# Kernel tuning notes

Measured on AMD Instinct MI355X. Metric: run time of the kernel, lower is better.

## Reference

```python
import jax, jax.numpy as jnp
import numpy as np

EMBED_DICT = 200
EMBED_DIM = 16
HIDDEN = 32
LSTM_DIM = 256
B, C, L = 8192, 16, 64
END_IDX = 1  # stand-in for token_list.index('<End>')


def _lin(k, i, o):
    return jax.random.normal(k, (i, o), jnp.float32) * (1.0 / np.sqrt(i))


def setup_inputs() -> dict:
    key = jax.random.key(0)
    ks = jax.random.split(key, 20)
    feat_in = EMBED_DIM * 14 + LSTM_DIM  # 480
    z = lambda n: jnp.zeros((n,), jnp.float32)
    return {
        "trees": jax.random.randint(ks[0], (B, 1 + C, 17), 0, L),
        "lstm_out_list": jax.random.normal(ks[1], (B, L, 1, LSTM_DIM), jnp.float32),
        "first_notes": jax.random.normal(ks[2], (B, EMBED_DIM), jnp.float32),
        "train": 1,
        "embedding": jax.random.normal(ks[3], (EMBED_DICT, EMBED_DIM), jnp.float32) * 0.05,
        "leaf_end_W": _lin(ks[4], EMBED_DIM, HIDDEN), "leaf_end_b": z(HIDDEN),
        "lc_W1": _lin(ks[5], feat_in, HIDDEN * 4), "lc_b1": z(HIDDEN * 4),
        "lc_W2": _lin(ks[6], HIDDEN * 4, HIDDEN), "lc_b2": z(HIDDEN),
        "cs_W1": _lin(ks[7], HIDDEN * 2, HIDDEN * 4), "cs_b1": z(HIDDEN * 4),
        "cs_W2": _lin(ks[8], HIDDEN * 4, HIDDEN), "cs_b2": z(HIDDEN),
        "nf_W1": _lin(ks[9], feat_in, HIDDEN * 4), "nf_b1": z(HIDDEN * 4),
        "nf_W2": _lin(ks[10], HIDDEN * 4, HIDDEN), "nf_b2": z(HIDDEN),
        "cb_W1": _lin(ks[11], HIDDEN * 2, HIDDEN * 4), "cb_b1": z(HIDDEN * 4),
        "cb_W2": _lin(ks[12], HIDDEN * 4, HIDDEN), "cb_b2": z(HIDDEN),
        "ff_W1": _lin(ks[13], HIDDEN, HIDDEN), "ff_b1": z(HIDDEN),
        "ff_W2": _lin(ks[14], HIDDEN, HIDDEN), "ff_b2": z(HIDDEN),
        "ts_W": _lin(ks[15], HIDDEN, 1), "ts_b": z(1),
    }


def _mlp2(x, W1, b1, W2, b2):
    # Linear -> ReLU -> Linear -> ReLU (matches nn.Sequential blocks)
    return jax.nn.relu(jax.nn.relu(x @ W1 + b1) @ W2 + b2)


def reference(trees, lstm_out_list, first_notes, train, embedding,
              leaf_end_W, leaf_end_b, lc_W1, lc_b1, lc_W2, lc_b2,
              cs_W1, cs_b1, cs_W2, cs_b2, nf_W1, nf_b1, nf_W2, nf_b2,
              cb_W1, cb_b1, cb_W2, cb_b2, ff_W1, ff_b1, ff_W2, ff_b2,
              ts_W, ts_b):
    Bn = trees.shape[0]
    root = trees[:, 0, :]        # (B, 17)
    leaves = trees[:, 1:, :]     # (B, C, 17)
    Cn = leaves.shape[1]
    bidx = jnp.arange(Bn)

    # ---- leaf nodes: either leaf_end_ff(embed(type)) or leaf_child_ff(concat) ----
    leaf_tok = embedding[leaves[:, :, 2:-1]].reshape(Bn, Cn, -1)       # (B,C,224)
    leaf_ptr = lstm_out_list[bidx[:, None], leaves[:, :, -1], 0, :]    # (B,C,256)
    leaf_child = _mlp2(jnp.concatenate([leaf_tok, leaf_ptr], -1),
                       lc_W1, lc_b1, lc_W2, lc_b2)                     # (B,C,32)
    leaf_end = embedding[leaves[:, :, 2]] @ leaf_end_W + leaf_end_b    # (B,C,32)
    is_end = (leaves[:, :, 2] == END_IDX)[..., None]
    children = jnp.where(is_end, leaf_end, leaf_child)                 # (B,C,32)

    # ---- sequential left fold with child_sum_ff over children ----
    def step(carry, child):
        nxt = _mlp2(jnp.concatenate([carry, child], -1), cs_W1, cs_b1, cs_W2, cs_b2)
        return nxt, None
    child_summary, _ = jax.lax.scan(step, children[:, 0],
                                    jnp.moveaxis(children[:, 1:], 0, 1))  # (B,32)

    # ---- root node embedding + combine ----
    node_tok = embedding[root[:, 2:-1]].reshape(Bn, -1)                # (B,224)
    node_ptr = lstm_out_list[bidx, root[:, -1], 0, :]                  # (B,256)
    node_tmp = _mlp2(jnp.concatenate([node_tok, node_ptr], -1),
                     nf_W1, nf_b1, nf_W2, nf_b2)                       # (B,32)
    tree_sum = _mlp2(jnp.concatenate([node_tmp, child_summary], -1),
                     cb_W1, cb_b1, cb_W2, cb_b2)                       # (B,32)

    # ---- head: two linears (no activation) then score ----
    ff = (tree_sum @ ff_W1 + ff_b1) @ ff_W2 + ff_b2
    return ff @ ts_W + ts_b                                            # (B,1)
```

## Files before the change

### kernel.cpp

```cpp
#include <hip/hip_runtime.h>
#include <cstddef>


typedef __bf16 bf16x8 __attribute__((ext_vector_type(8)));
typedef __bf16 bf16x4 __attribute__((ext_vector_type(4)));
typedef float  f32x4  __attribute__((ext_vector_type(4)));

__global__ __launch_bounds__(256) void prep_kernel(
    const float* __restrict__ embedding,
    const float* __restrict__ leaf_end_W, const float* __restrict__ leaf_end_b,
    const float* __restrict__ lc_W1, const float* __restrict__ lc_W2,
    const float* __restrict__ nf_W1, const float* __restrict__ nf_W2,
    const float* __restrict__ cs_W1, const float* __restrict__ cs_W2,
    const float* __restrict__ cb_W1, const float* __restrict__ cb_W2,
    const float* __restrict__ ff_W1, const float* __restrict__ ff_b1,
    const float* __restrict__ ff_W2, const float* __restrict__ ff_b2,
    const float* __restrict__ ts_W, const float* __restrict__ ts_b,
    __bf16* __restrict__ lcW1T, __bf16* __restrict__ nfW1T,
    __bf16* __restrict__ lcW2T, __bf16* __restrict__ nfW2T,
    __bf16* __restrict__ emb_bf, float* __restrict__ endvec,
    __bf16* __restrict__ csW1Th, __bf16* __restrict__ csW1Tl,
    __bf16* __restrict__ cbW1Th, __bf16* __restrict__ cbW1Tl,
    __bf16* __restrict__ csW2Th, __bf16* __restrict__ csW2Tl,
    __bf16* __restrict__ cbW2Th, __bf16* __restrict__ cbW2Tl,
    float* __restrict__ vfin, float* __restrict__ cfin)
{
    const int id = blockIdx.x * 256 + threadIdx.x;
    if (id < 61440) {
        const int n = id / 480, k = id - n * 480;
        lcW1T[id] = (__bf16)lc_W1[k * 128 + n];
    } else if (id < 122880) {
        const int e = id - 61440;
        const int n = e / 480, k = e - n * 480;
        nfW1T[e] = (__bf16)nf_W1[k * 128 + n];
    } else if (id < 126976) {
        const int e = id - 122880;
        const int n = e / 128, k = e - n * 128;
        lcW2T[e] = (__bf16)lc_W2[k * 32 + n];
    } else if (id < 131072) {
        const int e = id - 126976;
        const int n = e / 128, k = e - n * 128;
        nfW2T[e] = (__bf16)nf_W2[k * 32 + n];
    } else if (id < 134272) {
        emb_bf[id - 131072] = (__bf16)embedding[id - 131072];
    } else if (id < 134304) {
        const int c = id - 134272;
        float a = leaf_end_b[c];
        #pragma unroll
        for (int d = 0; d < 16; ++d) a = fmaf(embedding[16 + d], leaf_end_W[d * 32 + c], a);
        endvec[c] = a;
    } else if (id < 142496) {
        const int e = id - 134304;
        const int n = e >> 6, k = e & 63;
        const float v = cs_W1[k * 128 + n];
        const __bf16 h = (__bf16)v;
        csW1Th[e] = h; csW1Tl[e] = (__bf16)(v - (float)h);
    } else if (id < 150688) {
        const int e = id - 142496;
        const int n = e >> 6, k = e & 63;
        const float v = cb_W1[k * 128 + n];
        const __bf16 h = (__bf16)v;
        cbW1Th[e] = h; cbW1Tl[e] = (__bf16)(v - (float)h);
    } else if (id < 154784) {
        const int e = id - 150688;
        const int n = e >> 7, k = e & 127;
        const float v = cs_W2[k * 32 + n];
        const __bf16 h = (__bf16)v;
        csW2Th[e] = h; csW2Tl[e] = (__bf16)(v - (float)h);
    } else if (id < 158880) {
        const int e = id - 154784;
        const int n = e >> 7, k = e & 127;
        const float v = cb_W2[k * 32 + n];
        const __bf16 h = (__bf16)v;
        cbW2Th[e] = h; cbW2Tl[e] = (__bf16)(v - (float)h);
    } else if (id < 158912) {
        const int c = id - 158880;
        float w2t[32];
        #pragma unroll
        for (int k = 0; k < 32; ++k) {
            float a = 0.f;
            for (int j = 0; j < 32; ++j) a = fmaf(ff_W2[k * 32 + j], ts_W[j], a);
            w2t[k] = a;
        }
        float a = 0.f;
        #pragma unroll
        for (int k = 0; k < 32; ++k) a = fmaf(ff_W1[c * 32 + k], w2t[k], a);
        vfin[c] = a;
    } else if (id == 158912) {
        float a = ts_b[0];
        for (int j = 0; j < 32; ++j) a = fmaf(ff_b2[j], ts_W[j], a);
        for (int k = 0; k < 32; ++k) {
            float w2t = 0.f;
            for (int j = 0; j < 32; ++j) w2t = fmaf(ff_W2[k * 32 + j], ts_W[j], w2t);
            a = fmaf(ff_b1[k], w2t, a);
        }
        cfin[0] = a;
    }
}

__global__ __launch_bounds__(256, 4) void mlp1_mfma(
    const int* __restrict__ trees,
    const float* __restrict__ lstm,
    const __bf16* __restrict__ lcW1T, const __bf16* __restrict__ nfW1T,
    const __bf16* __restrict__ lcW2T, const __bf16* __restrict__ nfW2T,
    const __bf16* __restrict__ emb_bf, const float* __restrict__ endvec,
    const float* __restrict__ lc_b1, const float* __restrict__ lc_b2,
    const float* __restrict__ nf_b1, const float* __restrict__ nf_b2,
    __bf16* __restrict__ childrenH, __bf16* __restrict__ childrenL,
    __bf16* __restrict__ node_tmpH, __bf16* __restrict__ node_tmpL)
{
    __shared__ __align__(16) __bf16 emb_s[3200];
    __shared__ __align__(16) __bf16 Hs[64][136];
    __shared__ float b1s[128], b2s[32], evs[32];
    __shared__ int   endf[64];

    const int tid = threadIdx.x;
    const int blk = blockIdx.x;
    const bool leaf = (blk < 2048);

    const __bf16* __restrict__ W1T = leaf ? lcW1T : nfW1T;
    const __bf16* __restrict__ W2T = leaf ? lcW2T : nfW2T;
    const float*  __restrict__ b1p = leaf ? lc_b1 : nf_b1;
    const float*  __restrict__ b2p = leaf ? lc_b2 : nf_b2;

    for (int i = tid; i < 3200; i += 256) emb_s[i] = emb_bf[i];
    if (tid < 128) b1s[tid] = b1p[tid];
    if (tid < 32)  { b2s[tid] = b2p[tid]; evs[tid] = leaf ? endvec[tid] : 0.f; }
    if (tid < 64) {
        if (leaf) {
            const int R = blk * 64 + tid;
            const int b = R >> 4, trow = 1 + (R & 15);
            endf[tid] = (trees[(b * 17 + trow) * 17 + 2] == 1);
        } else endf[tid] = 0;
    }

    const int l  = tid & 63;
    const int w  = tid >> 6;
    const int wm = w >> 1;
    const int wn = w & 1;
    const int lm = l & 15;
    const int kb = l >> 4;

    const int* tb[2];
    const float* lb[2];
    #pragma unroll
    for (int i = 0; i < 2; ++i) {
        const int r = wm * 32 + i * 16 + lm;
        int b, trow;
        if (leaf) { const int R = blk * 64 + r; b = R >> 4; trow = 1 + (R & 15); }
        else      { b = (blk - 2048) * 64 + r; trow = 0; }
        const int* t = trees + (b * 17 + trow) * 17;
        tb[i] = t;
        lb[i] = lstm + ((size_t)b * 64 + (size_t)t[16]) * 256;
    }

    f32x4 acc[2][4];
    #pragma unroll
    for (int i = 0; i < 2; ++i)
        #pragma unroll
        for (int j = 0; j < 4; ++j) acc[i][j] = (f32x4){0.f, 0.f, 0.f, 0.f};

    __syncthreads();

    #pragma unroll
    for (int c = 0; c < 15; ++c) {
        bf16x8 bfr[4];
        #pragma unroll
        for (int ct = 0; ct < 4; ++ct) {
            const int n = wn * 64 + ct * 16 + lm;
            bfr[ct] = *(const bf16x8*)(W1T + n * 480 + c * 32 + kb * 8);
        }
        bf16x8 afr[2];
        if (c < 7) {
            #pragma unroll
            for (int i = 0; i < 2; ++i) {
                const int tok = tb[i][2 + 2 * c + (kb >> 1)];
                afr[i] = *(const bf16x8*)(emb_s + tok * 16 + (kb & 1) * 8);
            }
        } else {
            #pragma unroll
            for (int i = 0; i < 2; ++i) {
                const float* p = lb[i] + (c - 7) * 32 + kb * 8;
                const float4 u = *(const float4*)p;
                const float4 v = *(const float4*)(p + 4);
                bf16x8 t;
                t[0] = (__bf16)u.x; t[1] = (__bf16)u.y; t[2] = (__bf16)u.z; t[3] = (__bf16)u.w;
                t[4] = (__bf16)v.x; t[5] = (__bf16)v.y; t[6] = (__bf16)v.z; t[7] = (__bf16)v.w;
                afr[i] = t;
            }
        }
        #pragma unroll
        for (int i = 0; i < 2; ++i)
            #pragma unroll
            for (int ct = 0; ct < 4; ++ct)
                acc[i][ct] = __builtin_amdgcn_mfma_f32_16x16x32_bf16(afr[i], bfr[ct], acc[i][ct], 0, 0, 0);
    }

    #pragma unroll
    for (int i = 0; i < 2; ++i)
        #pragma unroll
        for (int ct = 0; ct < 4; ++ct) {
            const int col = wn * 64 + ct * 16 + lm;
            const float bias = b1s[col];
            #pragma unroll
            for (int rg = 0; rg < 4; ++rg) {
                float v = acc[i][ct][rg] + bias;
                v = v > 0.f ? v : 0.f;
                Hs[wm * 32 + i * 16 + 4 * kb + rg][col] = (__bf16)v;
            }
        }
    __syncthreads();

    f32x4 acc2[2];
    acc2[0] = (f32x4){0.f, 0.f, 0.f, 0.f};
    acc2[1] = (f32x4){0.f, 0.f, 0.f, 0.f};

    #pragma unroll
    for (int kc = 0; kc < 4; ++kc) {
        const bf16x8 a2 = *(const bf16x8*)(&Hs[w * 16 + lm][kc * 32 + kb * 8]);
        #pragma unroll
        for (int j = 0; j < 2; ++j) {
            const bf16x8 b2 = *(const bf16x8*)(W2T + (j * 16 + lm) * 128 + kc * 32 + kb * 8);
            acc2[j] = __builtin_amdgcn_mfma_f32_16x16x32_bf16(a2, b2, acc2[j], 0, 0, 0);
        }
    }

    #pragma unroll
    for (int j = 0; j < 2; ++j) {
        const int col = j * 16 + lm;
        const float bias = b2s[col];
        #pragma unroll
        for (int rg = 0; rg < 4; ++rg) {
            const int row = w * 16 + 4 * kb + rg;
            float v = acc2[j][rg] + bias;
            v = v > 0.f ? v : 0.f;
            if (leaf && endf[row]) v = evs[col];
            const __bf16 h  = (__bf16)v;
            const __bf16 lo = (__bf16)(v - (float)h);
            if (leaf) {
                const size_t R = (size_t)blk * 64 + row;
                childrenH[R * 32 + col] = h;
                childrenL[R * 32 + col] = lo;
            } else {
                const size_t R = (size_t)(blk - 2048) * 64 + row;
                node_tmpH[R * 32 + col] = h;
                node_tmpL[R * 32 + col] = lo;
            }
        }
    }
}

__global__ __launch_bounds__(256) void scan_mfma(
    const __bf16* __restrict__ childrenH, const __bf16* __restrict__ childrenL,
    const __bf16* __restrict__ node_tmpH, const __bf16* __restrict__ node_tmpL,
    const __bf16* __restrict__ csW1Th, const __bf16* __restrict__ csW1Tl,
    const __bf16* __restrict__ csW2Th, const __bf16* __restrict__ csW2Tl,
    const __bf16* __restrict__ cbW1Th, const __bf16* __restrict__ cbW1Tl,
    const __bf16* __restrict__ cbW2Th, const __bf16* __restrict__ cbW2Tl,
    const float* __restrict__ cs_b1, const float* __restrict__ cs_b2,
    const float* __restrict__ cb_b1, const float* __restrict__ cb_b2,
    const float* __restrict__ vfin_g, const float* __restrict__ cfin_g,
    float* __restrict__ out)
{
    __shared__ __align__(16) __bf16 Xh[32][72], Xl[32][72];
    __shared__ __align__(16) __bf16 Hh[32][136], Hl[32][136];
    __shared__ float b1a[128], b1b[128], b2a[32], b2b[32], vfin[32];
    __shared__ float psum[2][32];
    __shared__ float cfin_s;

    const int tid = threadIdx.x;
    const int l = tid & 63, w = tid >> 6;
    const int lm = l & 15, kb = l >> 4;

    if (tid < 128)      { b1a[tid] = cs_b1[tid]; b1b[tid] = cb_b1[tid]; }
    else if (tid < 160) { b2a[tid - 128] = cs_b2[tid - 128]; b2b[tid - 128] = cb_b2[tid - 128]; }
    else if (tid < 192) { vfin[tid - 160] = vfin_g[tid - 160]; }
    else if (tid == 192) cfin_s = cfin_g[0];

    bf16x8 W1r[2][2][2];
    {
        #pragma unroll
        for (int nt = 0; nt < 2; ++nt)
            #pragma unroll
            for (int kc = 0; kc < 2; ++kc) {
                const int n = w * 32 + nt * 16 + lm;
                W1r[nt][kc][0] = *(const bf16x8*)(csW1Th + n * 64 + kc * 32 + kb * 8);
                W1r[nt][kc][1] = *(const bf16x8*)(csW1Tl + n * 64 + kc * 32 + kb * 8);
            }
    }
    bf16x8 W2r[4][2];
    {
        const int n2 = (w & 1) * 16 + lm;
        #pragma unroll
        for (int kc = 0; kc < 4; ++kc) {
            W2r[kc][0] = *(const bf16x8*)(csW2Th + n2 * 128 + kc * 32 + kb * 8);
            W2r[kc][1] = *(const bf16x8*)(csW2Tl + n2 * 128 + kc * 32 + kb * 8);
        }
    }

    const size_t base = (size_t)blockIdx.x * 32;
    const int tt = tid >> 3, c4 = (tid & 7) * 4;

    {
        const size_t o0 = ((base + tt) * 16 + 0) * 32 + c4;
        const size_t o1 = ((base + tt) * 16 + 1) * 32 + c4;
        *(bf16x4*)&Xh[tt][c4]      = *(const bf16x4*)(childrenH + o0);
        *(bf16x4*)&Xl[tt][c4]      = *(const bf16x4*)(childrenL + o0);
        *(bf16x4*)&Xh[tt][32 + c4] = *(const bf16x4*)(childrenH + o1);
        *(bf16x4*)&Xl[tt][32 + c4] = *(const bf16x4*)(childrenL + o1);
    }
    __syncthreads();

    #pragma unroll 1
    for (int it = 1; it <= 16; ++it) {
        const bool fin = (it == 16);
        if (fin) {
            #pragma unroll
            for (int nt = 0; nt < 2; ++nt)
                #pragma unroll
                for (int kc = 0; kc < 2; ++kc) {
                    const int n = w * 32 + nt * 16 + lm;
                    W1r[nt][kc][0] = *(const bf16x8*)(cbW1Th + n * 64 + kc * 32 + kb * 8);
                    W1r[nt][kc][1] = *(const bf16x8*)(cbW1Tl + n * 64 + kc * 32 + kb * 8);
                }
            const int n2 = (w & 1) * 16 + lm;
            #pragma unroll
            for (int kc = 0; kc < 4; ++kc) {
                W2r[kc][0] = *(const bf16x8*)(cbW2Th + n2 * 128 + kc * 32 + kb * 8);
                W2r[kc][1] = *(const bf16x8*)(cbW2Tl + n2 * 128 + kc * 32 + kb * 8);
            }
        }
        const float* __restrict__ b1c = fin ? b1b : b1a;
        const float* __restrict__ b2c = fin ? b2b : b2a;

        bf16x4 pfh, pfl;
        const int pfmode = (it < 15) ? 1 : (it == 15 ? 2 : 0);
        if (pfmode == 1) {
            const size_t o = ((base + tt) * 16 + (it + 1)) * 32 + c4;
            pfh = *(const bf16x4*)(childrenH + o);
            pfl = *(const bf16x4*)(childrenL + o);
        } else if (pfmode == 2) {
            const size_t o = (base + tt) * 32 + c4;
            pfh = *(const bf16x4*)(node_tmpH + o);
            pfl = *(const bf16x4*)(node_tmpL + o);
        }

        bf16x8 xh[2][2], xl[2][2];
        #pragma unroll
        for (int i = 0; i < 2; ++i)
            #pragma unroll
            for (int kc = 0; kc < 2; ++kc) {
                const int row = i * 16 + lm;
                xh[i][kc] = *(const bf16x8*)&Xh[row][kc * 32 + kb * 8];
                xl[i][kc] = *(const bf16x8*)&Xl[row][kc * 32 + kb * 8];
            }
        f32x4 a1[2][2];
        #pragma unroll
        for (int i = 0; i < 2; ++i)
            #pragma unroll
            for (int nt = 0; nt < 2; ++nt) {
                a1[i][nt] = (f32x4){0.f, 0.f, 0.f, 0.f};
                #pragma unroll
                for (int kc = 0; kc < 2; ++kc) {
                    a1[i][nt] = __builtin_amdgcn_mfma_f32_16x16x32_bf16(xh[i][kc], W1r[nt][kc][0], a1[i][nt], 0, 0, 0);
                    a1[i][nt] = __builtin_amdgcn_mfma_f32_16x16x32_bf16(xl[i][kc], W1r[nt][kc][0], a1[i][nt], 0, 0, 0);
                    a1[i][nt] = __builtin_amdgcn_mfma_f32_16x16x32_bf16(xh[i][kc], W1r[nt][kc][1], a1[i][nt], 0, 0, 0);
                }
            }
        #pragma unroll
        for (int i = 0; i < 2; ++i)
            #pragma unroll
            for (int nt = 0; nt < 2; ++nt) {
                const int col = w * 32 + nt * 16 + lm;
                const float bias = b1c[col];
                #pragma unroll
                for (int rg = 0; rg < 4; ++rg) {
                    const int row = i * 16 + 4 * kb + rg;
                    float v = a1[i][nt][rg] + bias;
                    v = v > 0.f ? v : 0.f;
                    const __bf16 h = (__bf16)v;
                    Hh[row][col] = h;
                    Hl[row][col] = (__bf16)(v - (float)h);
                }
            }
        __syncthreads();

        const int mt = w >> 1;
        f32x4 a2 = (f32x4){0.f, 0.f, 0.f, 0.f};
        #pragma unroll
        for (int kc = 0; kc < 4; ++kc) {
            const bf16x8 ah = *(const bf16x8*)&Hh[mt * 16 + lm][kc * 32 + kb * 8];
            const bf16x8 al = *(const bf16x8*)&Hl[mt * 16 + lm][kc * 32 + kb * 8];
            a2 = __builtin_amdgcn_mfma_f32_16x16x32_bf16(ah, W2r[kc][0], a2, 0, 0, 0);
            a2 = __builtin_amdgcn_mfma_f32_16x16x32_bf16(al, W2r[kc][0], a2, 0, 0, 0);
            a2 = __builtin_amdgcn_mfma_f32_16x16x32_bf16(ah, W2r[kc][1], a2, 0, 0, 0);
        }

        if (!fin) {
            const int cb_ = (it == 15) ? 32 : 0;
            const int col = (w & 1) * 16 + lm;
            const float bias = b2c[col];
            #pragma unroll
            for (int rg = 0; rg < 4; ++rg) {
                const int row = mt * 16 + 4 * kb + rg;
                float v = a2[rg] + bias;
                v = v > 0.f ? v : 0.f;
                const __bf16 h = (__bf16)v;
                Xh[row][cb_ + col] = h;
                Xl[row][cb_ + col] = (__bf16)(v - (float)h);
            }
            if (pfmode) {
                const int dst = (pfmode == 2) ? 0 : 32;
                *(bf16x4*)&Xh[tt][dst + c4] = pfh;
                *(bf16x4*)&Xl[tt][dst + c4] = pfl;
            }
            __syncthreads();
        } else {
            const int col = (w & 1) * 16 + lm;
            const float bias = b2c[col];
            const float vf = vfin[col];
            float part[4];
            #pragma unroll
            for (int rg = 0; rg < 4; ++rg) {
                float v = a2[rg] + bias;
                v = v > 0.f ? v : 0.f;
                part[rg] = v * vf;
            }
            #pragma unroll
            for (int m = 1; m < 16; m <<= 1)
                #pragma unroll
                for (int rg = 0; rg < 4; ++rg)
                    part[rg] += __shfl_xor(part[rg], m, 64);
            if (lm == 0) {
                #pragma unroll
                for (int rg = 0; rg < 4; ++rg)
                    psum[w & 1][mt * 16 + 4 * kb + rg] = part[rg];
            }
            __syncthreads();
            if (tid < 32) out[base + tid] = cfin_s + psum[0][tid] + psum[1][tid];
        }
    }
}

extern "C" void kernel_launch(void* const* d_in, const int* in_sizes, int n_in,
                              void* d_out, int out_size, void* d_ws, size_t ws_size,
                              hipStream_t stream) {
    const int*   trees      = (const int*)d_in[0];
    const float* lstm       = (const float*)d_in[1];
    const float* embedding  = (const float*)d_in[4];
    const float* leaf_end_W = (const float*)d_in[5];
    const float* leaf_end_b = (const float*)d_in[6];
    const float* lc_W1 = (const float*)d_in[7];
    const float* lc_b1 = (const float*)d_in[8];
    const float* lc_W2 = (const float*)d_in[9];
    const float* lc_b2 = (const float*)d_in[10];
    const float* cs_W1 = (const float*)d_in[11];
    const float* cs_b1 = (const float*)d_in[12];
    const float* cs_W2 = (const float*)d_in[13];
    const float* cs_b2 = (const float*)d_in[14];
    const float* nf_W1 = (const float*)d_in[15];
    const float* nf_b1 = (const float*)d_in[16];
    const float* nf_W2 = (const float*)d_in[17];
    const float* nf_b2 = (const float*)d_in[18];
    const float* cb_W1 = (const float*)d_in[19];
    const float* cb_b1 = (const float*)d_in[20];
    const float* cb_W2 = (const float*)d_in[21];
    const float* cb_b2 = (const float*)d_in[22];
    const float* ff_W1 = (const float*)d_in[23];
    const float* ff_b1 = (const float*)d_in[24];
    const float* ff_W2 = (const float*)d_in[25];
    const float* ff_b2 = (const float*)d_in[26];
    const float* ts_W  = (const float*)d_in[27];
    const float* ts_b  = (const float*)d_in[28];

    char* ws = (char*)d_ws;
    __bf16* childrenH = (__bf16*)ws;
    __bf16* childrenL = (__bf16*)(ws + 8388608);
    __bf16* node_tmpH = (__bf16*)(ws + 16777216);
    __bf16* node_tmpL = (__bf16*)(ws + 17301504);
    __bf16* lcW1T    = (__bf16*)(ws + 17825792);
    __bf16* nfW1T    = (__bf16*)(ws + 17948672);
    __bf16* lcW2T    = (__bf16*)(ws + 18071552);
    __bf16* nfW2T    = (__bf16*)(ws + 18079744);
    __bf16* emb_bf   = (__bf16*)(ws + 18087936);
    float*  endvec   = (float*)(ws + 18094336);
    __bf16* csW1Th   = (__bf16*)(ws + 18094464);
    __bf16* csW1Tl   = (__bf16*)(ws + 18110848);
    __bf16* cbW1Th   = (__bf16*)(ws + 18127232);
    __bf16* cbW1Tl   = (__bf16*)(ws + 18143616);
    __bf16* csW2Th   = (__bf16*)(ws + 18160000);
    __bf16* csW2Tl   = (__bf16*)(ws + 18168192);
    __bf16* cbW2Th   = (__bf16*)(ws + 18176384);
    __bf16* cbW2Tl   = (__bf16*)(ws + 18184576);
    float*  vfin     = (float*)(ws + 18192768);
    float*  cfin     = (float*)(ws + 18192896);
    float*  outp     = (float*)d_out;

    prep_kernel<<<dim3(621), dim3(256), 0, stream>>>(
        embedding, leaf_end_W, leaf_end_b, lc_W1, lc_W2, nf_W1, nf_W2,
        cs_W1, cs_W2, cb_W1, cb_W2, ff_W1, ff_b1, ff_W2, ff_b2, ts_W, ts_b,
        lcW1T, nfW1T, lcW2T, nfW2T, emb_bf, endvec,
        csW1Th, csW1Tl, cbW1Th, cbW1Tl, csW2Th, csW2Tl, cbW2Th, cbW2Tl,
        vfin, cfin);

    mlp1_mfma<<<dim3(2176), dim3(256), 0, stream>>>(
        trees, lstm, lcW1T, nfW1T, lcW2T, nfW2T, emb_bf, endvec,
        lc_b1, lc_b2, nf_b1, nf_b2, childrenH, childrenL, node_tmpH, node_tmpL);

    scan_mfma<<<dim3(256), dim3(256), 0, stream>>>(
        childrenH, childrenL, node_tmpH, node_tmpL,
        csW1Th, csW1Tl, csW2Th, csW2Tl, cbW1Th, cbW1Tl, cbW2Th, cbW2Tl,
        cs_b1, cs_b2, cb_b1, cb_b2, vfin, cfin, outp);
}
```

Before: 129.3 us.

## Halve mlp1 tile rows, swap MFMA operands for packed stores, coalesce prep reads

```diff
diff --git a/kernel.cpp b/kernel.cpp
--- a/kernel.cpp
+++ b/kernel.cpp
@@ -27,20 +27,20 @@
 {
     const int id = blockIdx.x * 256 + threadIdx.x;
     if (id < 61440) {
-        const int n = id / 480, k = id - n * 480;
-        lcW1T[id] = (__bf16)lc_W1[k * 128 + n];
+        const int k = id >> 7, n = id & 127;
+        lcW1T[n * 480 + k] = (__bf16)lc_W1[id];
     } else if (id < 122880) {
         const int e = id - 61440;
-        const int n = e / 480, k = e - n * 480;
-        nfW1T[e] = (__bf16)nf_W1[k * 128 + n];
+        const int k = e >> 7, n = e & 127;
+        nfW1T[n * 480 + k] = (__bf16)nf_W1[e];
     } else if (id < 126976) {
         const int e = id - 122880;
-        const int n = e / 128, k = e - n * 128;
-        lcW2T[e] = (__bf16)lc_W2[k * 32 + n];
+        const int k = e >> 5, n = e & 31;
+        lcW2T[n * 128 + k] = (__bf16)lc_W2[e];
     } else if (id < 131072) {
         const int e = id - 126976;
-        const int n = e / 128, k = e - n * 128;
-        nfW2T[e] = (__bf16)nf_W2[k * 32 + n];
+        const int k = e >> 5, n = e & 31;
+        nfW2T[n * 128 + k] = (__bf16)nf_W2[e];
     } else if (id < 134272) {
         emb_bf[id - 131072] = (__bf16)embedding[id - 131072];
     } else if (id < 134304) {
@@ -51,28 +51,28 @@
         endvec[c] = a;
     } else if (id < 142496) {
         const int e = id - 134304;
-        const int n = e >> 6, k = e & 63;
-        const float v = cs_W1[k * 128 + n];
+        const int k = e >> 7, n = e & 127;
+        const float v = cs_W1[e];
         const __bf16 h = (__bf16)v;
-        csW1Th[e] = h; csW1Tl[e] = (__bf16)(v - (float)h);
+        csW1Th[n * 64 + k] = h; csW1Tl[n * 64 + k] = (__bf16)(v - (float)h);
     } else if (id < 150688) {
         const int e = id - 142496;
-        const int n = e >> 6, k = e & 63;
-        const float v = cb_W1[k * 128 + n];
+        const int k = e >> 7, n = e & 127;
+        const float v = cb_W1[e];
         const __bf16 h = (__bf16)v;
-        cbW1Th[e] = h; cbW1Tl[e] = (__bf16)(v - (float)h);
+        cbW1Th[n * 64 + k] = h; cbW1Tl[n * 64 + k] = (__bf16)(v - (float)h);
     } else if (id < 154784) {
         const int e = id - 150688;
-        const int n = e >> 7, k = e & 127;
-        const float v = cs_W2[k * 32 + n];
+        const int k = e >> 5, n = e & 31;
+        const float v = cs_W2[e];
         const __bf16 h = (__bf16)v;
-        csW2Th[e] = h; csW2Tl[e] = (__bf16)(v - (float)h);
+        csW2Th[n * 128 + k] = h; csW2Tl[n * 128 + k] = (__bf16)(v - (float)h);
     } else if (id < 158880) {
         const int e = id - 154784;
-        const int n = e >> 7, k = e & 127;
-        const float v = cb_W2[k * 32 + n];
+        const int k = e >> 5, n = e & 31;
+        const float v = cb_W2[e];
         const __bf16 h = (__bf16)v;
-        cbW2Th[e] = h; cbW2Tl[e] = (__bf16)(v - (float)h);
+        cbW2Th[n * 128 + k] = h; cbW2Tl[n * 128 + k] = (__bf16)(v - (float)h);
     } else if (id < 158912) {
         const int c = id - 158880;
         float w2t[32];
@@ -98,7 +98,7 @@
     }
 }
 
-__global__ __launch_bounds__(256, 4) void mlp1_mfma(
+__global__ __launch_bounds__(256, 6) void mlp1_mfma(
     const int* __restrict__ trees,
     const float* __restrict__ lstm,
     const __bf16* __restrict__ lcW1T, const __bf16* __restrict__ nfW1T,
@@ -110,13 +110,13 @@
     __bf16* __restrict__ node_tmpH, __bf16* __restrict__ node_tmpL)
 {
     __shared__ __align__(16) __bf16 emb_s[3200];
-    __shared__ __align__(16) __bf16 Hs[64][136];
+    __shared__ __align__(16) __bf16 Hs[32][136];
     __shared__ float b1s[128], b2s[32], evs[32];
-    __shared__ int   endf[64];
+    __shared__ int   endf[32];
 
     const int tid = threadIdx.x;
     const int blk = blockIdx.x;
-    const bool leaf = (blk < 2048);
+    const bool leaf = (blk < 4096);
 
     const __bf16* __restrict__ W1T = leaf ? lcW1T : nfW1T;
     const __bf16* __restrict__ W2T = leaf ? lcW2T : nfW2T;
@@ -126,9 +126,9 @@
     for (int i = tid; i < 3200; i += 256) emb_s[i] = emb_bf[i];
     if (tid < 128) b1s[tid] = b1p[tid];
     if (tid < 32)  { b2s[tid] = b2p[tid]; evs[tid] = leaf ? endvec[tid] : 0.f; }
-    if (tid < 64) {
+    if (tid < 32) {
         if (leaf) {
-            const int R = blk * 64 + tid;
+            const int R = blk * 32 + tid;
             const int b = R >> 4, trow = 1 + (R & 15);
             endf[tid] = (trees[(b * 17 + trow) * 17 + 2] == 1);
         } else endf[tid] = 0;
@@ -136,116 +136,95 @@
 
     const int l  = tid & 63;
     const int w  = tid >> 6;
-    const int wm = w >> 1;
-    const int wn = w & 1;
     const int lm = l & 15;
     const int kb = l >> 4;
-
-    const int* tb[2];
-    const float* lb[2];
+    const int rowbase = (w >> 1) * 16;
+    const int colbase = (w & 1) * 64;
+
+    const int row = rowbase + lm;
+    int b, trow;
+    if (leaf) { const int R = blk * 32 + row; b = R >> 4; trow = 1 + (R & 15); }
+    else      { b = (blk - 4096) * 32 + row; trow = 0; }
+    const int* __restrict__ ti = trees + (b * 17 + trow) * 17;
+    const float* __restrict__ lrow = lstm + ((size_t)b * 64 + (size_t)ti[16]) * 256;
+
+    f32x4 acc[4];
     #pragma unroll
-    for (int i = 0; i < 2; ++i) {
-        const int r = wm * 32 + i * 16 + lm;
-        int b, trow;
-        if (leaf) { const int R = blk * 64 + r; b = R >> 4; trow = 1 + (R & 15); }
-        else      { b = (blk - 2048) * 64 + r; trow = 0; }
-        const int* t = trees + (b * 17 + trow) * 17;
-        tb[i] = t;
-        lb[i] = lstm + ((size_t)b * 64 + (size_t)t[16]) * 256;
-    }
-
-    f32x4 acc[2][4];
-    #pragma unroll
-    for (int i = 0; i < 2; ++i)
-        #pragma unroll
-        for (int j = 0; j < 4; ++j) acc[i][j] = (f32x4){0.f, 0.f, 0.f, 0.f};
+    for (int j = 0; j < 4; ++j) acc[j] = (f32x4){0.f, 0.f, 0.f, 0.f};
 
     __syncthreads();
 
     #pragma unroll
     for (int c = 0; c < 15; ++c) {
-        bf16x8 bfr[4];
+        bf16x8 wfr[4];
         #pragma unroll
         for (int ct = 0; ct < 4; ++ct) {
-            const int n = wn * 64 + ct * 16 + lm;
-            bfr[ct] = *(const bf16x8*)(W1T + n * 480 + c * 32 + kb * 8);
-        }
-        bf16x8 afr[2];
+            const int n = colbase + ct * 16 + lm;
+            wfr[ct] = *(const bf16x8*)(W1T + n * 480 + c * 32 + kb * 8);
+        }
+        bf16x8 afr;
         if (c < 7) {
-            #pragma unroll
-            for (int i = 0; i < 2; ++i) {
-                const int tok = tb[i][2 + 2 * c + (kb >> 1)];
-                afr[i] = *(const bf16x8*)(emb_s + tok * 16 + (kb & 1) * 8);
-            }
+            const int tok = ti[2 + 2 * c + (kb >> 1)];
+            afr = *(const bf16x8*)(emb_s + tok * 16 + (kb & 1) * 8);
         } else {
-            #pragma unroll
-            for (int i = 0; i < 2; ++i) {
-                const float* p = lb[i] + (c - 7) * 32 + kb * 8;
-                const float4 u = *(const float4*)p;
-                const float4 v = *(const float4*)(p + 4);
-                bf16x8 t;
-                t[0] = (__bf16)u.x; t[1] = (__bf16)u.y; t[2] = (__bf16)u.z; t[3] = (__bf16)u.w;
-                t[4] = (__bf16)v.x; t[5] = (__bf16)v.y; t[6] = (__bf16)v.z; t[7] = (__bf16)v.w;
-                afr[i] = t;
-            }
-        }
-        #pragma unroll
-        for (int i = 0; i < 2; ++i)
-            #pragma unroll
-            for (int ct = 0; ct < 4; ++ct)
-                acc[i][ct] = __builtin_amdgcn_mfma_f32_16x16x32_bf16(afr[i], bfr[ct], acc[i][ct], 0, 0, 0);
+            const float* p = lrow + (c - 7) * 32 + kb * 8;
+            const float4 u = *(const float4*)p;
+            const float4 v = *(const float4*)(p + 4);
+            bf16x8 t;
+            t[0] = (__bf16)u.x; t[1] = (__bf16)u.y; t[2] = (__bf16)u.z; t[3] = (__bf16)u.w;
+            t[4] = (__bf16)v.x; t[5] = (__bf16)v.y; t[6] = (__bf16)v.z; t[7] = (__bf16)v.w;
+            afr = t;
+        }
+        #pragma unroll
+        for (int ct = 0; ct < 4; ++ct)
+            acc[ct] = __builtin_amdgcn_mfma_f32_16x16x32_bf16(wfr[ct], afr, acc[ct], 0, 0, 0);
     }
 
     #pragma unroll
-    for (int i = 0; i < 2; ++i)
-        #pragma unroll
-        for (int ct = 0; ct < 4; ++ct) {
-            const int col = wn * 64 + ct * 16 + lm;
-            const float bias = b1s[col];
-            #pragma unroll
-            for (int rg = 0; rg < 4; ++rg) {
-                float v = acc[i][ct][rg] + bias;
-                v = v > 0.f ? v : 0.f;
-                Hs[wm * 32 + i * 16 + 4 * kb + rg][col] = (__bf16)v;
-            }
-        }
+    for (int ct = 0; ct < 4; ++ct) {
+        const int wcol = colbase + ct * 16 + 4 * kb;
+        bf16x4 pk;
+        #pragma unroll
+        for (int rg = 0; rg < 4; ++rg) {
+            float v = acc[ct][rg] + b1s[wcol + rg];
+            v = v > 0.f ? v : 0.f;
+            pk[rg] = (__bf16)v;
+        }
+        *(bf16x4*)&Hs[rowbase + lm][wcol] = pk;
+    }
     __syncthreads();
 
-    f32x4 acc2[2];
-    acc2[0] = (f32x4){0.f, 0.f, 0.f, 0.f};
-    acc2[1] = (f32x4){0.f, 0.f, 0.f, 0.f};
-
+    const int mt = w >> 1, jn = w & 1;
+    f32x4 a2 = (f32x4){0.f, 0.f, 0.f, 0.f};
     #pragma unroll
     for (int kc = 0; kc < 4; ++kc) {
-        const bf16x8 a2 = *(const bf16x8*)(&Hs[w * 16 + lm][kc * 32 + kb * 8]);
-        #pragma unroll
-        for (int j = 0; j < 2; ++j) {
-            const bf16x8 b2 = *(const bf16x8*)(W2T + (j * 16 + lm) * 128 + kc * 32 + kb * 8);
-            acc2[j] = __builtin_amdgcn_mfma_f32_16x16x32_bf16(a2, b2, acc2[j], 0, 0, 0);
-        }
-    }
-
-    #pragma unroll
-    for (int j = 0; j < 2; ++j) {
-        const int col = j * 16 + lm;
-        const float bias = b2s[col];
+        const bf16x8 wf = *(const bf16x8*)(W2T + (jn * 16 + lm) * 128 + kc * 32 + kb * 8);
+        const bf16x8 hf = *(const bf16x8*)(&Hs[mt * 16 + lm][kc * 32 + kb * 8]);
+        a2 = __builtin_amdgcn_mfma_f32_16x16x32_bf16(wf, hf, a2, 0, 0, 0);
+    }
+
+    {
+        const int orow = mt * 16 + lm;
+        const int ocol = jn * 16 + 4 * kb;
+        const bool isend = leaf && endf[orow];
+        bf16x4 ph, pl;
         #pragma unroll
         for (int rg = 0; rg < 4; ++rg) {
-            const int row = w * 16 + 4 * kb + rg;
-            float v = acc2[j][rg] + bias;
+            float v = a2[rg] + b2s[ocol + rg];
             v = v > 0.f ? v : 0.f;
-            if (leaf && endf[row]) v = evs[col];
-            const __bf16 h  = (__bf16)v;
-            const __bf16 lo = (__bf16)(v - (float)h);
-            if (leaf) {
-                const size_t R = (size_t)blk * 64 + row;
-                childrenH[R * 32 + col] = h;
-                childrenL[R * 32 + col] = lo;
-            } else {
-                const size_t R = (size_t)(blk - 2048) * 64 + row;
-                node_tmpH[R * 32 + col] = h;
-                node_tmpL[R * 32 + col] = lo;
-            }
+            if (isend) v = evs[ocol + rg];
+            const __bf16 h = (__bf16)v;
+            ph[rg] = h;
+            pl[rg] = (__bf16)(v - (float)h);
+        }
+        if (leaf) {
+            const size_t R = (size_t)blk * 32 + orow;
+            *(bf16x4*)&childrenH[R * 32 + ocol] = ph;
+            *(bf16x4*)&childrenL[R * 32 + ocol] = pl;
+        } else {
+            const size_t R = (size_t)(blk - 4096) * 32 + orow;
+            *(bf16x4*)&node_tmpH[R * 32 + ocol] = ph;
+            *(bf16x4*)&node_tmpL[R * 32 + ocol] = pl;
         }
     }
 }
@@ -278,16 +257,14 @@
     else if (tid == 192) cfin_s = cfin_g[0];
 
     bf16x8 W1r[2][2][2];
-    {
-        #pragma unroll
-        for (int nt = 0; nt < 2; ++nt)
-            #pragma unroll
-            for (int kc = 0; kc < 2; ++kc) {
-                const int n = w * 32 + nt * 16 + lm;
-                W1r[nt][kc][0] = *(const bf16x8*)(csW1Th + n * 64 + kc * 32 + kb * 8);
-                W1r[nt][kc][1] = *(const bf16x8*)(csW1Tl + n * 64 + kc * 32 + kb * 8);
-            }
-    }
+    #pragma unroll
+    for (int nt = 0; nt < 2; ++nt)
+        #pragma unroll
+        for (int kc = 0; kc < 2; ++kc) {
+            const int n = w * 32 + nt * 16 + lm;
+            W1r[nt][kc][0] = *(const bf16x8*)(csW1Th + n * 64 + kc * 32 + kb * 8);
+            W1r[nt][kc][1] = *(const bf16x8*)(csW1Tl + n * 64 + kc * 32 + kb * 8);
+        }
     bf16x8 W2r[4][2];
     {
         const int n2 = (w & 1) * 16 + lm;
@@ -347,68 +324,69 @@
 
         bf16x8 xh[2][2], xl[2][2];
         #pragma unroll
-        for (int i = 0; i < 2; ++i)
+        for (int tn = 0; tn < 2; ++tn)
             #pragma unroll
             for (int kc = 0; kc < 2; ++kc) {
-                const int row = i * 16 + lm;
-                xh[i][kc] = *(const bf16x8*)&Xh[row][kc * 32 + kb * 8];
-                xl[i][kc] = *(const bf16x8*)&Xl[row][kc * 32 + kb * 8];
+                xh[tn][kc] = *(const bf16x8*)&Xh[tn * 16 + lm][kc * 32 + kb * 8];
+                xl[tn][kc] = *(const bf16x8*)&Xl[tn * 16 + lm][kc * 32 + kb * 8];
             }
         f32x4 a1[2][2];
         #pragma unroll
-        for (int i = 0; i < 2; ++i)
+        for (int tn = 0; tn < 2; ++tn)
             #pragma unroll
             for (int nt = 0; nt < 2; ++nt) {
-                a1[i][nt] = (f32x4){0.f, 0.f, 0.f, 0.f};
+                a1[tn][nt] = (f32x4){0.f, 0.f, 0.f, 0.f};
                 #pragma unroll
                 for (int kc = 0; kc < 2; ++kc) {
-                    a1[i][nt] = __builtin_amdgcn_mfma_f32_16x16x32_bf16(xh[i][kc], W1r[nt][kc][0], a1[i][nt], 0, 0, 0);
-                    a1[i][nt] = __builtin_amdgcn_mfma_f32_16x16x32_bf16(xl[i][kc], W1r[nt][kc][0], a1[i][nt], 0, 0, 0);
-                    a1[i][nt] = __builtin_amdgcn_mfma_f32_16x16x32_bf16(xh[i][kc], W1r[nt][kc][1], a1[i][nt], 0, 0, 0);
+                    a1[tn][nt] = __builtin_amdgcn_mfma_f32_16x16x32_bf16(W1r[nt][kc][0], xh[tn][kc], a1[tn][nt], 0, 0, 0);
+                    a1[tn][nt] = __builtin_amdgcn_mfma_f32_16x16x32_bf16(W1r[nt][kc][0], xl[tn][kc], a1[tn][nt], 0, 0, 0);
+                    a1[tn][nt] = __builtin_amdgcn_mfma_f32_16x16x32_bf16(W1r[nt][kc][1], xh[tn][kc], a1[tn][nt], 0, 0, 0);
                 }
             }
         #pragma unroll
-        for (int i = 0; i < 2; ++i)
+        for (int tn = 0; tn < 2; ++tn)
             #pragma unroll
             for (int nt = 0; nt < 2; ++nt) {
-                const int col = w * 32 + nt * 16 + lm;
-                const float bias = b1c[col];
+                const int wcol = w * 32 + nt * 16 + 4 * kb;
+                bf16x4 ph, pl;
                 #pragma unroll
                 for (int rg = 0; rg < 4; ++rg) {
-                    const int row = i * 16 + 4 * kb + rg;
-                    float v = a1[i][nt][rg] + bias;
+                    float v = a1[tn][nt][rg] + b1c[wcol + rg];
                     v = v > 0.f ? v : 0.f;
                     const __bf16 h = (__bf16)v;
-                    Hh[row][col] = h;
-                    Hl[row][col] = (__bf16)(v - (float)h);
+                    ph[rg] = h;
+                    pl[rg] = (__bf16)(v - (float)h);
                 }
+                *(bf16x4*)&Hh[tn * 16 + lm][wcol] = ph;
+                *(bf16x4*)&Hl[tn * 16 + lm][wcol] = pl;
             }
         __syncthreads();
 
-        const int mt = w >> 1;
+        const int mt = w >> 1, jn = w & 1;
         f32x4 a2 = (f32x4){0.f, 0.f, 0.f, 0.f};
         #pragma unroll
         for (int kc = 0; kc < 4; ++kc) {
-            const bf16x8 ah = *(const bf16x8*)&Hh[mt * 16 + lm][kc * 32 + kb * 8];
-            const bf16x8 al = *(const bf16x8*)&Hl[mt * 16 + lm][kc * 32 + kb * 8];
-            a2 = __builtin_amdgcn_mfma_f32_16x16x32_bf16(ah, W2r[kc][0], a2, 0, 0, 0);
-            a2 = __builtin_amdgcn_mfma_f32_16x16x32_bf16(al, W2r[kc][0], a2, 0, 0, 0);
-            a2 = __builtin_amdgcn_mfma_f32_16x16x32_bf16(ah, W2r[kc][1], a2, 0, 0, 0);
+            const bf16x8 hh = *(const bf16x8*)&Hh[mt * 16 + lm][kc * 32 + kb * 8];
+            const bf16x8 hl = *(const bf16x8*)&Hl[mt * 16 + lm][kc * 32 + kb * 8];
+            a2 = __builtin_amdgcn_mfma_f32_16x16x32_bf16(W2r[kc][0], hh, a2, 0, 0, 0);
+            a2 = __builtin_amdgcn_mfma_f32_16x16x32_bf16(W2r[kc][0], hl, a2, 0, 0, 0);
+            a2 = __builtin_amdgcn_mfma_f32_16x16x32_bf16(W2r[kc][1], hh, a2, 0, 0, 0);
         }
 
         if (!fin) {
             const int cb_ = (it == 15) ? 32 : 0;
-            const int col = (w & 1) * 16 + lm;
-            const float bias = b2c[col];
+            const int ocol = jn * 16 + 4 * kb;
+            bf16x4 ph, pl;
             #pragma unroll
             for (int rg = 0; rg < 4; ++rg) {
-                const int row = mt * 16 + 4 * kb + rg;
-                float v = a2[rg] + bias;
+                float v = a2[rg] + b2c[ocol + rg];
                 v = v > 0.f ? v : 0.f;
                 const __bf16 h = (__bf16)v;
-                Xh[row][cb_ + col] = h;
-                Xl[row][cb_ + col] = (__bf16)(v - (float)h);
-            }
+                ph[rg] = h;
+                pl[rg] = (__bf16)(v - (float)h);
+            }
+            *(bf16x4*)&Xh[mt * 16 + lm][cb_ + ocol] = ph;
+            *(bf16x4*)&Xl[mt * 16 + lm][cb_ + ocol] = pl;
             if (pfmode) {
                 const int dst = (pfmode == 2) ? 0 : 32;
                 *(bf16x4*)&Xh[tt][dst + c4] = pfh;
@@ -416,26 +394,17 @@
             }
             __syncthreads();
         } else {
-            const int col = (w & 1) * 16 + lm;
-            const float bias = b2c[col];
-            const float vf = vfin[col];
-            float part[4];
+            const int ocol = jn * 16 + 4 * kb;
+            float p = 0.f;
             #pragma unroll
             for (int rg = 0; rg < 4; ++rg) {
-                float v = a2[rg] + bias;
+                float v = a2[rg] + b2c[ocol + rg];
                 v = v > 0.f ? v : 0.f;
-                part[rg] = v * vf;
-            }
-            #pragma unroll
-            for (int m = 1; m < 16; m <<= 1)
-                #pragma unroll
-                for (int rg = 0; rg < 4; ++rg)
-                    part[rg] += __shfl_xor(part[rg], m, 64);
-            if (lm == 0) {
-                #pragma unroll
-                for (int rg = 0; rg < 4; ++rg)
-                    psum[w & 1][mt * 16 + 4 * kb + rg] = part[rg];
-            }
+                p = fmaf(v, vfin[ocol + rg], p);
+            }
+            p += __shfl_xor(p, 16, 64);
+            p += __shfl_xor(p, 32, 64);
+            if (kb == 0) psum[jn][mt * 16 + lm] = p;
             __syncthreads();
             if (tid < 32) out[base + tid] = cfin_s + psum[0][tid] + psum[1][tid];
         }
@@ -503,7 +472,7 @@
         csW1Th, csW1Tl, cbW1Th, cbW1Tl, csW2Th, csW2Tl, cbW2Th, cbW2Tl,
         vfin, cfin);
 
-    mlp1_mfma<<<dim3(2176), dim3(256), 0, stream>>>(
+    mlp1_mfma<<<dim3(4352), dim3(256), 0, stream>>>(
         trees, lstm, lcW1T, nfW1T, lcW2T, nfW2T, emb_bf, endvec,
         lc_b1, lc_b2, nf_b1, nf_b2, childrenH, childrenL, node_tmpH, node_tmpL);
 
```

Result: slower. 150.0 us (+16.0%).
